# Kernel tuning notes

Hardware: AMD Instinct MI355X
Metric: run time of the kernel (lower is better)

The kernel has to match this reference:

```python
import jax, jax.numpy as jnp
import numpy as np

jax.config.update("jax_enable_x64", True)  # hash math uses int64, matching torch promotion

NUM_LEVELS = 16
MIN_RES = 16
MAX_RES = 1024
LOG2_T = 19
T = 2 ** LOG2_T          # hash table size per level
FEATS = 2                # features per level
HASH_INIT_SCALE = 0.001
N = 524288               # number of query points

# 8 cube corners; bit==1 selects ceil coordinate (weight = offset), bit==0 selects floor (weight = 1-offset)
CORNER_BITS = np.array([[(b >> 2) & 1, (b >> 1) & 1, b & 1] for b in range(8)], dtype=np.int64)
PRIMES = np.array([1, 2654435761, 805459861], dtype=np.int64)


def setup_inputs() -> dict:
    key = jax.random.key(0)
    k1, k2 = jax.random.split(key)
    x = jax.random.uniform(k1, (N, 3), dtype=jnp.float32, minval=-1.0, maxval=1.0)
    hash_table = (jax.random.uniform(k2, (T * NUM_LEVELS, FEATS), dtype=jnp.float32) * 2.0 - 1.0) * HASH_INIT_SCALE
    return {"x": x, "hash_table": hash_table}


def reference(x, hash_table):
    # per-level resolutions: floor(min_res * growth^level)
    growth = np.exp((np.log(MAX_RES) - np.log(MIN_RES)) / (NUM_LEVELS - 1))
    scalings = jnp.asarray(np.floor(MIN_RES * growth ** np.arange(NUM_LEVELS)), dtype=jnp.float32)  # [L]
    hash_offset = jnp.arange(NUM_LEVELS, dtype=jnp.int64) * T  # [L]

    x01 = x * 0.5 + 0.5                                # map [-1,1] -> [0,1]
    scaled = x01[..., None, :] * scalings[:, None]     # [N, L, 3]
    sc = jnp.ceil(scaled).astype(jnp.int64)            # [N, L, 3]
    sf = jnp.floor(scaled).astype(jnp.int64)           # [N, L, 3]
    offset = scaled - sf.astype(scaled.dtype)          # [N, L, 3] in [0,1)

    bits = jnp.asarray(CORNER_BITS)                    # [8, 3]
    # corner integer coords: [N, L, 8, 3]
    corners = jnp.where(bits[None, None] == 1, sc[:, :, None, :], sf[:, :, None, :])

    # Instant-NGP spatial hash (int64, matching torch's type promotion)
    p = corners * jnp.asarray(PRIMES)
    h = jnp.bitwise_xor(jnp.bitwise_xor(p[..., 0], p[..., 1]), p[..., 2])
    h = h % T + hash_offset[None, :, None]             # [N, L, 8]

    # trilinear weights: prod over dims of (offset if ceil else 1-offset)
    w = jnp.prod(jnp.where(bits[None, None] == 1, offset[:, :, None, :], 1.0 - offset[:, :, None, :]), axis=-1)  # [N, L, 8]

    feats = hash_table[h]                              # [N, L, 8, F] gather
    enc = jnp.sum(feats * w[..., None], axis=-2)       # [N, L, F]
    return enc.reshape(*enc.shape[:-2], NUM_LEVELS * FEATS)  # [N, L*F]
```

## Files before the change

### kernel.cpp

```cpp
#include <hip/hip_runtime.h>
#include <cmath>

#define TBL_SIZE (1u << 19)
#define TBL_MASK (TBL_SIZE - 1u)
#define PRIME1 2654435761u
#define PRIME2 805459861u
#define NUM_LEVELS 16
#define DLMAX 7
#define PPB 32

struct Args {
    float s[NUM_LEVELS];
    uint32_t doff[DLMAX];
    int ddim[DLMAX];
};

typedef float v2f __attribute__((ext_vector_type(2)));

template<int CTRL>
__device__ __forceinline__ float dpp_add(float v) {
    int i = __builtin_bit_cast(int, v);
    int j = __builtin_amdgcn_mov_dpp(i, CTRL, 0xF, 0xF, true);
    return v + __builtin_bit_cast(float, j);
}

__device__ __forceinline__ uint32_t f2bf(float f) {
    uint32_t u = __builtin_bit_cast(uint32_t, f);
    return (u + 0x7FFFu + ((u >> 16) & 1u)) >> 16;
}
__device__ __forceinline__ float bflo(uint32_t v) { return __builtin_bit_cast(float, v << 16); }
__device__ __forceinline__ float bfhi(uint32_t v) { return __builtin_bit_cast(float, v & 0xFFFF0000u); }

__global__ __launch_bounds__(256) void cvt_hashed_kernel(
    const float* __restrict__ table, uint32_t* __restrict__ dst, int DL, int nentries)
{
    int gid = blockIdx.x * 256 + (int)threadIdx.x;
    if (gid >= nentries) return;
    float2 e = reinterpret_cast<const float2*>(table)[((size_t)DL << 19) + gid];
    dst[gid] = f2bf(e.x) | (f2bf(e.y) << 16);
}

__global__ __launch_bounds__(256) void build_dense_kernel(
    const float* __restrict__ table, uint32_t* __restrict__ dst,
    uint32_t doff, int dim, int level, int nentries)
{
    int id = blockIdx.x * 256 + (int)threadIdx.x;
    if (id >= nentries) return;
    int d2 = dim * dim;
    int xp = id / d2; int rem = id - xp * d2;
    int yp = rem / dim; int zp = rem - yp * dim;
    uint32_t h = (uint32_t)xp ^ ((uint32_t)yp * PRIME1) ^ ((uint32_t)zp * PRIME2);
    float2 e = reinterpret_cast<const float2*>(table)[((size_t)level << 19) + (h & TBL_MASK)];
    dst[doff + id] = f2bf(e.x) | (f2bf(e.y) << 16);
}

__global__ __launch_bounds__(256) void HashEncoding_88837103551034_kernel(
    const float* __restrict__ x,
    const float* __restrict__ table,
    const uint32_t* __restrict__ ws32,
    float* __restrict__ out,
    int npoints, int CH, int perXcdHard, int hardTotal, int easyTotal,
    int DL, int NBF, uint32_t bfbase,
    Args args)
{
    int b = blockIdx.x; int xcd = b & 7; int sb = b >> 3;
    int t = (int)threadIdx.x;
    int corner = t & 7;

    int level, chunk;
    if (sb < perXcdHard) {
        int g = xcd * perXcdHard + sb;
        if (g >= hardTotal) return;
        int li = g / CH; chunk = g - li * CH;
        if (DL == DLMAX) level = (li == 0) ? 6 : 6 + li;
        else             level = DL + li;
    } else {
        int g = (sb - perXcdHard) * 8 + xcd;
        if (g >= easyTotal) return;
        int li = g / CH; chunk = g - li * CH;
        level = li;
    }

    int n = chunk * PPB + (t >> 3);
    if (n >= npoints) return;

    float x0 = x[(size_t)n * 3 + 0] * 0.5f + 0.5f;
    float x1 = x[(size_t)n * 3 + 1] * 0.5f + 0.5f;
    float x2 = x[(size_t)n * 3 + 2] * 0.5f + 0.5f;
    float sl = args.s[level];
    float sx = x0 * sl, sy = x1 * sl, sz = x2 * sl;
    float fx = floorf(sx), fy = floorf(sy), fz = floorf(sz);
    float ox = sx - fx, oy = sy - fy, oz = sz - fz;
    int bx = (corner >> 2) & 1, by = (corner >> 1) & 1, bz = corner & 1;

    float f0, f1;
    if (level < DL) {
        int dim = args.ddim[level];
        int idx = (((int)fx + bx) * dim + (int)fy + by) * dim + (int)fz + bz;
        uint32_t v = ws32[args.doff[level] + idx];
        f0 = bflo(v); f1 = bfhi(v);
    } else {
        uint32_t h = (uint32_t)((int)fx + bx)
                   ^ ((uint32_t)((int)fy + by) * PRIME1)
                   ^ ((uint32_t)((int)fz + bz) * PRIME2);
        uint32_t idx = h & TBL_MASK;
        int li = level - DL;
        if (li < NBF) {
            uint32_t v = ws32[bfbase + ((size_t)li << 19) + idx];
            f0 = bflo(v); f1 = bfhi(v);
        } else {
            float2 f = reinterpret_cast<const float2*>(table)[((size_t)level << 19) + idx];
            f0 = f.x; f1 = f.y;
        }
    }

    float w = (bx ? ox : 1.f - ox) * (by ? oy : 1.f - oy) * (bz ? oz : 1.f - oz);
    float e0 = f0 * w, e1 = f1 * w;
    e0 = dpp_add<0xB1>(e0);  e1 = dpp_add<0xB1>(e1);
    e0 = dpp_add<0x4E>(e0);  e1 = dpp_add<0x4E>(e1);
    e0 = dpp_add<0x141>(e0); e1 = dpp_add<0x141>(e1);
    if (corner == 0) {
        v2f res; res.x = e0; res.y = e1;
        __builtin_nontemporal_store(res, (v2f*)(out + (size_t)n * 32 + level * 2));
    }
}

extern "C" void kernel_launch(void* const* d_in, const int* in_sizes, int n_in,
                              void* d_out, int out_size, void* d_ws, size_t ws_size,
                              hipStream_t stream) {
    const float* x = (const float*)d_in[0];
    const float* table = (const float*)d_in[1];
    float* out = (float*)d_out;
    int npoints = in_sizes[0] / 3;

    Args args;
    double growth = std::exp((std::log(1024.0) - std::log(16.0)) / 15.0);
    for (int l = 0; l < NUM_LEVELS; ++l)
        args.s[l] = (float)std::floor(16.0 * std::pow(growth, (double)l));
    for (int l = 0; l < DLMAX; ++l) { args.doff[l] = 0; args.ddim[l] = 1; }

    uint64_t cum4 = 0; int DL = 0;
    int nent_d[DLMAX];
    for (int l = 0; l < DLMAX; ++l) {
        int dim = (int)args.s[l] + 2;
        uint64_t ent = (uint64_t)dim * dim * dim;
        if ((cum4 + ent) * 4 > ws_size) break;
        args.doff[l] = (uint32_t)cum4; args.ddim[l] = dim;
        nent_d[l] = (int)ent;
        cum4 += ent; DL = l + 1;
    }
    uint64_t used = cum4 * 4;
    int NBF = 0; uint32_t bfbase = (uint32_t)cum4;
    if (ws_size > used) {
        NBF = (int)((ws_size - used) / ((uint64_t)TBL_SIZE * 4));
        if (NBF > NUM_LEVELS - DL) NBF = NUM_LEVELS - DL;
    }

    uint32_t* ws32 = (uint32_t*)d_ws;
    if (NBF > 0) {
        int nent = NBF << 19;
        cvt_hashed_kernel<<<(nent + 255) / 256, 256, 0, stream>>>(table, ws32 + bfbase, DL, nent);
    }
    for (int l = 0; l < DL; ++l) {
        build_dense_kernel<<<(nent_d[l] + 255) / 256, 256, 0, stream>>>(
            table, ws32, args.doff[l], args.ddim[l], l, nent_d[l]);
    }

    int CH = (npoints + PPB - 1) / PPB;
    int elvls = (DL > 6) ? 6 : DL;
    int hardUnits = (NUM_LEVELS - DL) + (DL == DLMAX ? 1 : 0);
    int hardTotal = hardUnits * CH;
    int easyTotal = elvls * CH;
    int perXcdHard = (hardTotal + 7) / 8;
    int perXcdEasy = (easyTotal + 7) / 8;
    int grid = 8 * (perXcdHard + perXcdEasy);

    HashEncoding_88837103551034_kernel<<<grid, 256, 0, stream>>>(
        x, table, ws32, out, npoints, CH, perXcdHard, hardTotal, easyTotal,
        DL, NBF, bfbase, args);
}
```

Measured before the change: 272.1 us.

## Serve three coarsest levels from LDS-resident dense grids in a persistent kernel

The three coarsest levels (dims 17/22/28, about 128 KB of bf16-packed entries) are built into a compact dense table. A persistent 1024-thread kernel loads that table into LDS and computes those levels from shared memory. The remaining 13 levels use the bf16 hashed copies in a simplified hash kernel, and dense grids for levels 3-6 are dropped. This trades the cheaper dense lookups of levels 3-6 for hashed gathers, adds a separate kernel launch, and requires 128 KB of LDS per block, which limits occupancy to one block per CU.

```diff
diff --git a/kernel.cpp b/kernel.cpp
--- a/kernel.cpp
+++ b/kernel.cpp
@@ -6,14 +6,18 @@
 #define PRIME1 2654435761u
 #define PRIME2 805459861u
 #define NUM_LEVELS 16
-#define DLMAX 7
 #define PPB 32
 
-struct Args {
-    float s[NUM_LEVELS];
-    uint32_t doff[DLMAX];
-    int ddim[DLMAX];
-};
+#define D0g 17
+#define D1g 22
+#define D2g 28
+#define NW0 (D0g*D0g*D0g)
+#define NW1 (D1g*D1g*D1g)
+#define NW2 (D2g*D2g*D2g)
+#define NWTOT (NW0+NW1+NW2)
+#define LDSB (NWTOT*4)
+
+struct Args { float s[NUM_LEVELS]; };
 
 typedef float v2f __attribute__((ext_vector_type(2)));
 
@@ -32,55 +36,91 @@
 __device__ __forceinline__ float bfhi(uint32_t v) { return __builtin_bit_cast(float, v & 0xFFFF0000u); }
 
 __global__ __launch_bounds__(256) void cvt_hashed_kernel(
-    const float* __restrict__ table, uint32_t* __restrict__ dst, int DL, int nentries)
+    const float* __restrict__ table, uint32_t* __restrict__ dst, int L0, int nentries)
 {
     int gid = blockIdx.x * 256 + (int)threadIdx.x;
     if (gid >= nentries) return;
-    float2 e = reinterpret_cast<const float2*>(table)[((size_t)DL << 19) + gid];
+    float2 e = reinterpret_cast<const float2*>(table)[((size_t)L0 << 19) + gid];
     dst[gid] = f2bf(e.x) | (f2bf(e.y) << 16);
 }
 
-__global__ __launch_bounds__(256) void build_dense_kernel(
-    const float* __restrict__ table, uint32_t* __restrict__ dst,
-    uint32_t doff, int dim, int level, int nentries)
+__global__ __launch_bounds__(256) void build_dense3_kernel(
+    const float* __restrict__ table, uint32_t* __restrict__ dst)
 {
     int id = blockIdx.x * 256 + (int)threadIdx.x;
-    if (id >= nentries) return;
-    int d2 = dim * dim;
-    int xp = id / d2; int rem = id - xp * d2;
-    int yp = rem / dim; int zp = rem - yp * dim;
+    if (id >= NWTOT) return;
+    int l, rel, D;
+    if (id < NW0)            { l = 0; rel = id;             D = D0g; }
+    else if (id < NW0 + NW1) { l = 1; rel = id - NW0;       D = D1g; }
+    else                     { l = 2; rel = id - NW0 - NW1; D = D2g; }
+    int d2 = D * D;
+    int xp = rel / d2; int rem = rel - xp * d2;
+    int yp = rem / D;  int zp = rem - yp * D;
     uint32_t h = (uint32_t)xp ^ ((uint32_t)yp * PRIME1) ^ ((uint32_t)zp * PRIME2);
-    float2 e = reinterpret_cast<const float2*>(table)[((size_t)level << 19) + (h & TBL_MASK)];
-    dst[doff + id] = f2bf(e.x) | (f2bf(e.y) << 16);
+    float2 e = reinterpret_cast<const float2*>(table)[((size_t)l << 19) + (h & TBL_MASK)];
+    dst[id] = f2bf(e.x) | (f2bf(e.y) << 16);
+}
+
+__global__ __launch_bounds__(1024) void lds_levels_kernel(
+    const float* __restrict__ x, const uint32_t* __restrict__ wsdense,
+    float* __restrict__ out, int npoints, int nchunks,
+    float s0, float s1, float s2)
+{
+    extern __shared__ uint32_t lds[];
+    for (int i = (int)threadIdx.x; i < NWTOT; i += 1024) lds[i] = wsdense[i];
+    __syncthreads();
+
+    const int t = (int)threadIdx.x;
+    const int corner = t & 7, p = t >> 3;
+    const int bx = (corner >> 2) & 1, by = (corner >> 1) & 1, bz = corner & 1;
+
+    for (int c = (int)blockIdx.x; c < nchunks; c += (int)gridDim.x) {
+        int n = c * 128 + p;
+        if (n < npoints) {
+            float x0 = x[(size_t)n * 3 + 0] * 0.5f + 0.5f;
+            float x1 = x[(size_t)n * 3 + 1] * 0.5f + 0.5f;
+            float x2 = x[(size_t)n * 3 + 2] * 0.5f + 0.5f;
+            const float ss[3] = {s0, s1, s2};
+            const int   dd[3] = {D0g, D1g, D2g};
+            const int   bb[3] = {0, NW0, NW0 + NW1};
+            #pragma unroll
+            for (int l = 0; l < 3; ++l) {
+                float sx = x0 * ss[l], sy = x1 * ss[l], sz = x2 * ss[l];
+                float fx = floorf(sx), fy = floorf(sy), fz = floorf(sz);
+                float ox = sx - fx, oy = sy - fy, oz = sz - fz;
+                int D = dd[l];
+                int idx = (((int)fx + bx) * D + (int)fy + by) * D + (int)fz + bz;
+                int mx = D * D * D - 1;
+                idx = idx < mx ? idx : mx;
+                uint32_t v = lds[bb[l] + idx];
+                float w = (bx ? ox : 1.f - ox) * (by ? oy : 1.f - oy) * (bz ? oz : 1.f - oz);
+                float e0 = bflo(v) * w, e1 = bfhi(v) * w;
+                e0 = dpp_add<0xB1>(e0);  e1 = dpp_add<0xB1>(e1);
+                e0 = dpp_add<0x4E>(e0);  e1 = dpp_add<0x4E>(e1);
+                e0 = dpp_add<0x141>(e0); e1 = dpp_add<0x141>(e1);
+                if (corner == 0) {
+                    v2f r; r.x = e0; r.y = e1;
+                    __builtin_nontemporal_store(r, (v2f*)(out + (size_t)n * 32 + l * 2));
+                }
+            }
+        }
+    }
 }
 
 __global__ __launch_bounds__(256) void HashEncoding_88837103551034_kernel(
     const float* __restrict__ x,
     const float* __restrict__ table,
-    const uint32_t* __restrict__ ws32,
+    const uint32_t* __restrict__ bfws,
     float* __restrict__ out,
-    int npoints, int CH, int perXcdHard, int hardTotal, int easyTotal,
-    int DL, int NBF, uint32_t bfbase,
+    int npoints, int CH, int perXcd, int total, int L0, int NBF,
     Args args)
 {
     int b = blockIdx.x; int xcd = b & 7; int sb = b >> 3;
+    int g = xcd * perXcd + sb;
+    if (g >= total) return;
+    int li = g / CH; int level = L0 + li; int chunk = g - li * CH;
     int t = (int)threadIdx.x;
     int corner = t & 7;
-
-    int level, chunk;
-    if (sb < perXcdHard) {
-        int g = xcd * perXcdHard + sb;
-        if (g >= hardTotal) return;
-        int li = g / CH; chunk = g - li * CH;
-        if (DL == DLMAX) level = (li == 0) ? 6 : 6 + li;
-        else             level = DL + li;
-    } else {
-        int g = (sb - perXcdHard) * 8 + xcd;
-        if (g >= easyTotal) return;
-        int li = g / CH; chunk = g - li * CH;
-        level = li;
-    }
-
     int n = chunk * PPB + (t >> 3);
     if (n >= npoints) return;
 
@@ -93,27 +133,19 @@
     float ox = sx - fx, oy = sy - fy, oz = sz - fz;
     int bx = (corner >> 2) & 1, by = (corner >> 1) & 1, bz = corner & 1;
 
+    uint32_t h = (uint32_t)((int)fx + bx)
+               ^ ((uint32_t)((int)fy + by) * PRIME1)
+               ^ ((uint32_t)((int)fz + bz) * PRIME2);
+    uint32_t idx = h & TBL_MASK;
+
     float f0, f1;
-    if (level < DL) {
-        int dim = args.ddim[level];
-        int idx = (((int)fx + bx) * dim + (int)fy + by) * dim + (int)fz + bz;
-        uint32_t v = ws32[args.doff[level] + idx];
+    if (li < NBF) {
+        uint32_t v = bfws[((size_t)li << 19) + idx];
         f0 = bflo(v); f1 = bfhi(v);
     } else {
-        uint32_t h = (uint32_t)((int)fx + bx)
-                   ^ ((uint32_t)((int)fy + by) * PRIME1)
-                   ^ ((uint32_t)((int)fz + bz) * PRIME2);
-        uint32_t idx = h & TBL_MASK;
-        int li = level - DL;
-        if (li < NBF) {
-            uint32_t v = ws32[bfbase + ((size_t)li << 19) + idx];
-            f0 = bflo(v); f1 = bfhi(v);
-        } else {
-            float2 f = reinterpret_cast<const float2*>(table)[((size_t)level << 19) + idx];
-            f0 = f.x; f1 = f.y;
-        }
-    }
-
+        float2 f = reinterpret_cast<const float2*>(table)[((size_t)level << 19) + idx];
+        f0 = f.x; f1 = f.y;
+    }
     float w = (bx ? ox : 1.f - ox) * (by ? oy : 1.f - oy) * (bz ? oz : 1.f - oz);
     float e0 = f0 * w, e1 = f1 * w;
     e0 = dpp_add<0xB1>(e0);  e1 = dpp_add<0xB1>(e1);
@@ -137,45 +169,33 @@
     double growth = std::exp((std::log(1024.0) - std::log(16.0)) / 15.0);
     for (int l = 0; l < NUM_LEVELS; ++l)
         args.s[l] = (float)std::floor(16.0 * std::pow(growth, (double)l));
-    for (int l = 0; l < DLMAX; ++l) { args.doff[l] = 0; args.ddim[l] = 1; }
-
-    uint64_t cum4 = 0; int DL = 0;
-    int nent_d[DLMAX];
-    for (int l = 0; l < DLMAX; ++l) {
-        int dim = (int)args.s[l] + 2;
-        uint64_t ent = (uint64_t)dim * dim * dim;
-        if ((cum4 + ent) * 4 > ws_size) break;
-        args.doff[l] = (uint32_t)cum4; args.ddim[l] = dim;
-        nent_d[l] = (int)ent;
-        cum4 += ent; DL = l + 1;
-    }
-    uint64_t used = cum4 * 4;
-    int NBF = 0; uint32_t bfbase = (uint32_t)cum4;
-    if (ws_size > used) {
-        NBF = (int)((ws_size - used) / ((uint64_t)TBL_SIZE * 4));
-        if (NBF > NUM_LEVELS - DL) NBF = NUM_LEVELS - DL;
-    }
-
+
+    int CH = (npoints + PPB - 1) / PPB;
     uint32_t* ws32 = (uint32_t*)d_ws;
-    if (NBF > 0) {
-        int nent = NBF << 19;
-        cvt_hashed_kernel<<<(nent + 255) / 256, 256, 0, stream>>>(table, ws32 + bfbase, DL, nent);
-    }
-    for (int l = 0; l < DL; ++l) {
-        build_dense_kernel<<<(nent_d[l] + 255) / 256, 256, 0, stream>>>(
-            table, ws32, args.doff[l], args.ddim[l], l, nent_d[l]);
-    }
-
-    int CH = (npoints + PPB - 1) / PPB;
-    int elvls = (DL > 6) ? 6 : DL;
-    int hardUnits = (NUM_LEVELS - DL) + (DL == DLMAX ? 1 : 0);
-    int hardTotal = hardUnits * CH;
-    int easyTotal = elvls * CH;
-    int perXcdHard = (hardTotal + 7) / 8;
-    int perXcdEasy = (easyTotal + 7) / 8;
-    int grid = 8 * (perXcdHard + perXcdEasy);
-
-    HashEncoding_88837103551034_kernel<<<grid, 256, 0, stream>>>(
-        x, table, ws32, out, npoints, CH, perXcdHard, hardTotal, easyTotal,
-        DL, NBF, bfbase, args);
-}
+
+    bool dimsOk = ((int)args.s[0] == 16) && ((int)args.s[1] == 21) && ((int)args.s[2] == 27);
+    size_t needA = ((size_t)13 * TBL_SIZE + (size_t)NWTOT) * 4;
+
+    if (dimsOk && ws_size >= needA) {
+        int nent = 13 << 19;
+        cvt_hashed_kernel<<<nent / 256, 256, 0, stream>>>(table, ws32, 3, nent);
+        uint32_t* wsdense = ws32 + (size_t)13 * TBL_SIZE;
+        build_dense3_kernel<<<(NWTOT + 255) / 256, 256, 0, stream>>>(table, wsdense);
+
+        hipFuncSetAttribute(reinterpret_cast<const void*>(lds_levels_kernel),
+                            hipFuncAttributeMaxDynamicSharedMemorySize, LDSB);
+        int nchunks = (npoints + 127) / 128;
+        lds_levels_kernel<<<256, 1024, LDSB, stream>>>(
+            x, wsdense, out, npoints, nchunks, args.s[0], args.s[1], args.s[2]);
+
+        int total = 13 * CH;
+        int perXcd = (total + 7) / 8;
+        HashEncoding_88837103551034_kernel<<<8 * perXcd, 256, 0, stream>>>(
+            x, table, ws32, out, npoints, CH, perXcd, total, 3, 13, args);
+    } else {
+        int total = 16 * CH;
+        int perXcd = (total + 7) / 8;
+        HashEncoding_88837103551034_kernel<<<8 * perXcd, 256, 0, stream>>>(
+            x, table, ws32, out, npoints, CH, perXcd, total, 0, 0, args);
+    }
+}
```

New measurement: 256.4 us. -5.8%, faster.
